# Optimization experiments

Hardware: AMD Instinct MI355X
Metric: run time of the kernel (lower is better)

## Reference

```python
import jax, jax.numpy as jnp
import numpy as np

K_DIM = 1024
HEADS = 16


def setup_inputs() -> dict:
    key = jax.random.key(0)
    ks = jax.random.split(key, 6)
    b, t, k = 2, 2048, K_DIM
    scale = 1.0 / np.sqrt(k)
    x = jax.random.normal(ks[0], (b, t, k), dtype=jnp.float32)
    # nn.Linear stores weight as [out, in]; y = x @ W.T
    Wq = jax.random.normal(ks[1], (k, k), dtype=jnp.float32) * scale
    Wk = jax.random.normal(ks[2], (k, k), dtype=jnp.float32) * scale
    Wv = jax.random.normal(ks[3], (k, k), dtype=jnp.float32) * scale
    Wo = jax.random.normal(ks[4], (k, k), dtype=jnp.float32) * scale
    bo = jax.random.normal(ks[5], (k,), dtype=jnp.float32) * scale
    return {"x": x, "Wq": Wq, "Wk": Wk, "Wv": Wv, "Wo": Wo, "bo": bo}


def reference(x, Wq, Wk, Wv, Wo, bo):
    b, t, k = x.shape
    h = HEADS
    hd = k // h
    q = (x @ Wq.T).reshape(b, t, h, hd)
    kk = (x @ Wk.T).reshape(b, t, h, hd)
    v = (x @ Wv.T).reshape(b, t, h, hd)
    # scores: [b, h, t, t]
    scores = jnp.einsum('bqhd,bkhd->bhqk', q, kk) / jnp.sqrt(jnp.float32(hd))
    w = jax.nn.softmax(scores, axis=-1)
    out = jnp.einsum('bhqk,bkhd->bqhd', w, v).reshape(b, t, k)
    return out @ Wo.T + bo
```

## Files before the change

### kernel.cpp

```cpp
#include <hip/hip_runtime.h>
#include <stdint.h>
#include <stddef.h>

#define TB 2048
#define KDIM 1024
#define NH 16
#define HD 64

typedef __attribute__((ext_vector_type(8))) __bf16 bf16x8;
typedef __attribute__((ext_vector_type(4))) float f32x4;
typedef __attribute__((ext_vector_type(16))) float f32x16;
typedef __attribute__((ext_vector_type(8))) unsigned short u16x8;
typedef __attribute__((ext_vector_type(4))) unsigned u32x4;
typedef __attribute__((ext_vector_type(2))) unsigned u32x2;

static __device__ __forceinline__ unsigned short f2bf(float f) {
  unsigned u = __builtin_bit_cast(unsigned, f);
  return (unsigned short)((u + 0x7FFFu + ((u >> 16) & 1u)) >> 16);
}

static __device__ __forceinline__ bf16x8 ld_frag(const unsigned short* p) {
  u16x8 v = *(const u16x8*)p;
  return __builtin_bit_cast(bf16x8, v);
}

static __device__ __forceinline__ void gload_lds16(const void* g, void* l) {
  auto gp = (const __attribute__((address_space(1))) unsigned int*)(uintptr_t)g;
  auto lp = (__attribute__((address_space(3))) unsigned int*)(unsigned int)(uintptr_t)l;
  __builtin_amdgcn_global_load_lds(gp, lp, 16, 0, 0);
}

static __device__ __forceinline__ float fast_exp2(float x) {
  float r;
  asm("v_exp_f32 %0, %1" : "=v"(r) : "v"(x));
  return r;
}

static __device__ __forceinline__ unsigned cvt_pk(float a, float b) {
  unsigned r;
  asm("v_cvt_pk_bf16_f32 %0, %1, %2" : "=v"(r) : "v"(a), "v"(b));
  return r;
}

static __device__ __forceinline__ u32x2 permswap(unsigned a, unsigned b) {
  return __builtin_amdgcn_permlane32_swap(a, b, false, false);
}

__global__ __launch_bounds__(256) void k_cvt_all(
    const float* __restrict__ x, const float* __restrict__ Wq,
    const float* __restrict__ Wk, const float* __restrict__ Wv,
    const float* __restrict__ Wo, unsigned short* __restrict__ xb,
    unsigned short* __restrict__ wb) {
  int bb = blockIdx.x;
  const float* src;
  unsigned short* dst;
  int i;
  if (bb < 2048) {
    src = x; dst = xb; i = bb * 256 + threadIdx.x;
  } else {
    int wsel = (bb - 2048) >> 9;
    src = (wsel == 0) ? Wq : (wsel == 1) ? Wk : (wsel == 2) ? Wv : Wo;
    dst = wb + (size_t)wsel * (KDIM * KDIM);
    i = ((bb - 2048) & 511) * 256 + threadIdx.x;
  }
  const float4* p = (const float4*)src + (size_t)i * 2;
  float4 a = p[0], b = p[1];
  u16x8 o;
  o[0] = f2bf(a.x); o[1] = f2bf(a.y); o[2] = f2bf(a.z); o[3] = f2bf(a.w);
  o[4] = f2bf(b.x); o[5] = f2bf(b.y); o[6] = f2bf(b.z); o[7] = f2bf(b.w);
  *((u16x8*)dst + i) = o;
}

template <int MODE>
static __device__ __forceinline__ void gemm_body(
    const unsigned short* __restrict__ A, const unsigned short* __restrict__ W,
    unsigned short* __restrict__ Cb, float* __restrict__ Cf,
    const float* __restrict__ bias, int by, int bx,
    unsigned short* As, unsigned short* Bs) {
  const int K = KDIM, N = KDIM;
  int tid = threadIdx.x, lane = tid & 63, wid = tid >> 6;
  int r = lane & 15, g = lane >> 4;
  int wm = wid >> 1, wn = wid & 1;

  f32x4 acc[4][4];
#pragma unroll
  for (int m = 0; m < 4; ++m)
#pragma unroll
    for (int n = 0; n < 4; ++n) acc[m][n] = (f32x4){0.f, 0.f, 0.f, 0.f};

  const unsigned short* Ag = A + (size_t)(by * 128) * K;
  const unsigned short* Wg = W + (size_t)(bx * 128) * K;

  for (int k0 = 0; k0 < K; k0 += 32) {
#pragma unroll
    for (int it = 0; it < 2; ++it) {
      int base = it * 256 + wid * 64;
      int c = base + lane;
      gload_lds16(Ag + (size_t)(c >> 2) * K + k0 + (c & 3) * 8, &As[base * 8]);
      gload_lds16(Wg + (size_t)(c >> 2) * K + k0 + (c & 3) * 8, &Bs[base * 8]);
    }
    __syncthreads();
    bf16x8 af[4], bf[4];
#pragma unroll
    for (int m = 0; m < 4; ++m) af[m] = ld_frag(&As[(wm * 64 + m * 16 + r) * 32 + g * 8]);
#pragma unroll
    for (int n = 0; n < 4; ++n) bf[n] = ld_frag(&Bs[(wn * 64 + n * 16 + r) * 32 + g * 8]);
#pragma unroll
    for (int m = 0; m < 4; ++m)
#pragma unroll
      for (int n = 0; n < 4; ++n)
        acc[m][n] = __builtin_amdgcn_mfma_f32_16x16x32_bf16(af[m], bf[n], acc[m][n], 0, 0, 0);
    __syncthreads();
  }

#pragma unroll
  for (int m = 0; m < 4; ++m)
#pragma unroll
    for (int n = 0; n < 4; ++n) {
      int col = bx * 128 + wn * 64 + n * 16 + r;
#pragma unroll
      for (int j = 0; j < 4; ++j) {
        int row = by * 128 + wm * 64 + m * 16 + g * 4 + j;
        if (MODE == 0)
          Cb[(size_t)row * N + col] = f2bf(acc[m][n][j]);
        else
          Cf[(size_t)row * N + col] = acc[m][n][j] + bias[col];
      }
    }
}

__global__ __launch_bounds__(256) void k_gemm_qkv(
    const unsigned short* __restrict__ X,
    const unsigned short* __restrict__ Wq, const unsigned short* __restrict__ Wk,
    const unsigned short* __restrict__ Wv,
    unsigned short* __restrict__ Q, unsigned short* __restrict__ Kp,
    unsigned short* __restrict__ V) {
  __shared__ __align__(16) unsigned short As[4096];
  __shared__ __align__(16) unsigned short Bs[4096];
  int idx = blockIdx.x;
  int by = idx / 24, bxx = idx % 24;
  int which = bxx >> 3, bx = bxx & 7;
  const unsigned short* W = (which == 0) ? Wq : (which == 1) ? Wk : Wv;
  unsigned short* C = (which == 0) ? Q : (which == 1) ? Kp : V;
  gemm_body<0>(X, W, C, nullptr, nullptr, by, bx, As, Bs);
}

__global__ __launch_bounds__(256) void k_gemm_out(
    const unsigned short* __restrict__ AO, const unsigned short* __restrict__ Wo,
    float* __restrict__ out, const float* __restrict__ bias) {
  __shared__ __align__(16) unsigned short As[4096];
  __shared__ __align__(16) unsigned short Bs[4096];
  int by = blockIdx.x >> 3, bx = blockIdx.x & 7;
  gemm_body<1>(AO, Wo, nullptr, out, bias, by, bx, As, Bs);
}

__global__ __launch_bounds__(256) void k_transpose_v(
    const unsigned short* __restrict__ V, unsigned short* __restrict__ Vt) {
  int tt = blockIdx.x & 31, bh = blockIdx.x >> 5;
  int b = bh >> 4, h = bh & 15;
  __shared__ __align__(16) unsigned short ls[64][72];
  int tid = threadIdx.x;
#pragma unroll
  for (int it = 0; it < 2; ++it) {
    int c = it * 256 + tid;
    int t = c >> 3, d0 = (c & 7) * 8;
    const unsigned short* src = V + ((size_t)(b * TB + tt * 64 + t)) * KDIM + h * HD + d0;
    *(u16x8*)&ls[t][d0] = *(const u16x8*)src;
  }
  __syncthreads();
#pragma unroll
  for (int it = 0; it < 2; ++it) {
    int c = it * 256 + tid;
    int d = c >> 3, t0 = (c & 7) * 8;
    u16x8 v;
#pragma unroll
    for (int j = 0; j < 8; ++j) v[j] = ls[t0 + j][d];
    unsigned short* dst = Vt + ((size_t)(bh * HD + d)) * TB + tt * 64 + t0;
    *(u16x8*)dst = v;
  }
}

__global__ __launch_bounds__(256) void k_attn(
    const unsigned short* __restrict__ Q, const unsigned short* __restrict__ Kp,
    const unsigned short* __restrict__ Vt, unsigned short* __restrict__ AO) {
  __shared__ __align__(16) unsigned short Ks[2][64 * 64];
  __shared__ __align__(16) unsigned short Vs[2][64 * 64];

  int qt = blockIdx.x & 15, bh = blockIdx.x >> 4;
  int b = bh >> 4, h = bh & 15;
  int tid = threadIdx.x, lane = tid & 63, w = tid >> 6;
  int q = lane & 31, hh = lane >> 5;
  const float LOG2E = 1.44269504f;
  const int NT = TB / 64;

  const unsigned short* Qp =
      Q + ((size_t)(b * TB + qt * 128 + w * 32 + q)) * KDIM + h * HD;
  bf16x8 qf[4];
#pragma unroll
  for (int f = 0; f < 4; ++f) qf[f] = ld_frag(&Qp[16 * f + 8 * hh]);

  f32x16 o0, o1;
#pragma unroll
  for (int i = 0; i < 16; ++i) { o0[i] = 0.f; o1[i] = 0.f; }
  float m_run = -1e30f, l_run = 0.f;

  const unsigned short* Kbase = Kp + (size_t)(b * TB) * KDIM + h * HD;
  const unsigned short* Vbase = Vt + (size_t)bh * HD * TB;

  auto stage = [&](int kt, int buf) {
#pragma unroll
    for (int it = 0; it < 2; ++it) {
      int base = it * 256 + w * 64;
      int c = base + lane;
      int rr = c >> 3;
      int blk = (c & 7) ^ (rr & 7);
      gload_lds16(Kbase + (size_t)(kt * 64 + rr) * KDIM + blk * 8, &Ks[buf][base * 8]);
      gload_lds16(Vbase + (size_t)rr * TB + kt * 64 + blk * 8, &Vs[buf][base * 8]);
    }
  };

  stage(0, 0);
  __syncthreads();
  int cur = 0;

  for (int kt = 0; kt < NT; ++kt) {
    if (kt + 1 < NT) stage(kt + 1, cur ^ 1);

    const unsigned short* Kc = &Ks[cur][0];
    f32x16 st[2];
    __builtin_amdgcn_s_setprio(1);
#pragma unroll
    for (int g = 0; g < 2; ++g) {
#pragma unroll
      for (int i = 0; i < 16; ++i) st[g][i] = 0.f;
#pragma unroll
      for (int f = 0; f < 4; ++f) {
        int row = g * 32 + q;
        int bl = (2 * f + hh) ^ (row & 7);
        bf16x8 kf = ld_frag(&Kc[row * 64 + bl * 8]);
        st[g] = __builtin_amdgcn_mfma_f32_32x32x16_bf16(kf, qf[f], st[g], 0, 0, 0);
      }
    }
    __builtin_amdgcn_s_setprio(0);

    float pm = -1e30f;
#pragma unroll
    for (int g = 0; g < 2; ++g)
#pragma unroll
      for (int i = 0; i < 16; ++i) pm = fmaxf(pm, st[g][i]);
    pm = fmaxf(pm, __shfl_xor(pm, 32));
    float spm = pm * 0.125f;
    if (!__all(spm <= m_run + 8.f)) {
      float mnew = fmaxf(m_run, spm);
      float sc = fast_exp2((m_run - mnew) * LOG2E);
      m_run = mnew;
      l_run *= sc;
#pragma unroll
      for (int p = 0; p < 16; ++p) {
        float scp = __shfl(sc, (p & 3) + 8 * (p >> 2) + 4 * hh);
        o0[p] *= scp;
        o1[p] *= scp;
      }
    }

    float c1 = 0.125f * LOG2E, c2 = m_run * LOG2E;
    float rs = 0.f;
    bf16x8 pa[4];
#pragma unroll
    for (int g = 0; g < 2; ++g) {
      float e[16];
#pragma unroll
      for (int i = 0; i < 16; ++i) {
        e[i] = fast_exp2(st[g][i] * c1 - c2);
        rs += e[i];
      }
      unsigned d[8];
#pragma unroll
      for (int i = 0; i < 8; ++i) d[i] = cvt_pk(e[2 * i], e[2 * i + 1]);
      u32x2 r1 = permswap(d[0], d[2]);
      u32x2 r2 = permswap(d[1], d[3]);
      u32x2 r3 = permswap(d[4], d[6]);
      u32x2 r4 = permswap(d[5], d[7]);
      u32x4 t0; t0[0] = r1.x; t0[1] = r2.x; t0[2] = r1.y; t0[3] = r2.y;
      u32x4 t1; t1[0] = r3.x; t1[1] = r4.x; t1[2] = r3.y; t1[3] = r4.y;
      pa[2 * g]     = __builtin_bit_cast(bf16x8, t0);
      pa[2 * g + 1] = __builtin_bit_cast(bf16x8, t1);
    }
    rs += __shfl_xor(rs, 32);
    l_run += rs;

    const unsigned short* Vc = &Vs[cur][0];
    __builtin_amdgcn_s_setprio(1);
#pragma unroll
    for (int s = 0; s < 4; ++s) {
      int bl = (2 * s + hh) ^ (q & 7);
      bf16x8 v0 = ld_frag(&Vc[q * 64 + bl * 8]);
      bf16x8 v1 = ld_frag(&Vc[(32 + q) * 64 + bl * 8]);
      o0 = __builtin_amdgcn_mfma_f32_32x32x16_bf16(pa[s], v0, o0, 0, 0, 0);
      o1 = __builtin_amdgcn_mfma_f32_32x32x16_bf16(pa[s], v1, o1, 0, 0, 0);
    }
    __builtin_amdgcn_s_setprio(0);

    __syncthreads();
    cur ^= 1;
  }

  float invl = 1.0f / l_run;
#pragma unroll
  for (int p = 0; p < 16; ++p) {
    int qr = (p & 3) + 8 * (p >> 2) + 4 * hh;
    float il = __shfl(invl, qr);
    int row = qt * 128 + w * 32 + qr;
    size_t base = ((size_t)(b * TB + row)) * KDIM + h * HD;
    AO[base + q]      = f2bf(o0[p] * il);
    AO[base + 32 + q] = f2bf(o1[p] * il);
  }
}

extern "C" void kernel_launch(void* const* d_in, const int* in_sizes, int n_in,
                              void* d_out, int out_size, void* d_ws, size_t ws_size,
                              hipStream_t stream) {
  const float* x  = (const float*)d_in[0];
  const float* Wq = (const float*)d_in[1];
  const float* Wk = (const float*)d_in[2];
  const float* Wv = (const float*)d_in[3];
  const float* Wo = (const float*)d_in[4];
  const float* bo = (const float*)d_in[5];

  char* ws = (char*)d_ws;
  const size_t MB = 1 << 20;
  unsigned short* xb  = (unsigned short*)(ws + 0 * MB);
  unsigned short* wqb = (unsigned short*)(ws + 8 * MB);
  unsigned short* wkb = (unsigned short*)(ws + 10 * MB);
  unsigned short* wvb = (unsigned short*)(ws + 12 * MB);
  unsigned short* wob = (unsigned short*)(ws + 14 * MB);
  unsigned short* Qb  = (unsigned short*)(ws + 16 * MB);
  unsigned short* Kb  = (unsigned short*)(ws + 24 * MB);
  unsigned short* Vb  = (unsigned short*)(ws + 32 * MB);
  unsigned short* Vtb = (unsigned short*)(ws + 40 * MB);
  unsigned short* AOb = (unsigned short*)(ws + 48 * MB);

  k_cvt_all<<<4096, 256, 0, stream>>>(x, Wq, Wk, Wv, Wo, xb, wqb);
  k_gemm_qkv<<<32 * 24, 256, 0, stream>>>(xb, wqb, wkb, wvb, Qb, Kb, Vb);
  k_transpose_v<<<1024, 256, 0, stream>>>(Vb, Vtb);
  k_attn<<<512, 256, 0, stream>>>(Qb, Kb, Vtb, AOb);
  k_gemm_out<<<256, 256, 0, stream>>>(AOb, wob, (float*)d_out, bo);
}
```

Before: 127.3 us.

## Split attention KV sequence across two wave groups per block and merge

```diff
diff --git a/kernel.cpp b/kernel.cpp
--- a/kernel.cpp
+++ b/kernel.cpp
@@ -180,21 +180,22 @@
   }
 }
 
-__global__ __launch_bounds__(256) void k_attn(
+__global__ __launch_bounds__(512, 4) void k_attn(
     const unsigned short* __restrict__ Q, const unsigned short* __restrict__ Kp,
     const unsigned short* __restrict__ Vt, unsigned short* __restrict__ AO) {
-  __shared__ __align__(16) unsigned short Ks[2][64 * 64];
-  __shared__ __align__(16) unsigned short Vs[2][64 * 64];
+  __shared__ __align__(16) unsigned short Ks[2][2][4096];
+  __shared__ __align__(16) unsigned short Vs[2][2][4096];
 
   int qt = blockIdx.x & 15, bh = blockIdx.x >> 4;
   int b = bh >> 4, h = bh & 15;
   int tid = threadIdx.x, lane = tid & 63, w = tid >> 6;
+  int wl = w & 3, half = w >> 2;
   int q = lane & 31, hh = lane >> 5;
   const float LOG2E = 1.44269504f;
-  const int NT = TB / 64;
+  const int HT = (TB / 64) / 2;
 
   const unsigned short* Qp =
-      Q + ((size_t)(b * TB + qt * 128 + w * 32 + q)) * KDIM + h * HD;
+      Q + ((size_t)(b * TB + qt * 128 + wl * 32 + q)) * KDIM + h * HD;
   bf16x8 qf[4];
 #pragma unroll
   for (int f = 0; f < 4; ++f) qf[f] = ld_frag(&Qp[16 * f + 8 * hh]);
@@ -210,23 +211,25 @@
   auto stage = [&](int kt, int buf) {
 #pragma unroll
     for (int it = 0; it < 2; ++it) {
-      int base = it * 256 + w * 64;
+      int base = it * 256 + wl * 64;
       int c = base + lane;
       int rr = c >> 3;
       int blk = (c & 7) ^ (rr & 7);
-      gload_lds16(Kbase + (size_t)(kt * 64 + rr) * KDIM + blk * 8, &Ks[buf][base * 8]);
-      gload_lds16(Vbase + (size_t)rr * TB + kt * 64 + blk * 8, &Vs[buf][base * 8]);
+      gload_lds16(Kbase + (size_t)(kt * 64 + rr) * KDIM + blk * 8,
+                  &Ks[half][buf][base * 8]);
+      gload_lds16(Vbase + (size_t)rr * TB + kt * 64 + blk * 8,
+                  &Vs[half][buf][base * 8]);
     }
   };
 
-  stage(0, 0);
+  stage(half * HT, 0);
   __syncthreads();
   int cur = 0;
 
-  for (int kt = 0; kt < NT; ++kt) {
-    if (kt + 1 < NT) stage(kt + 1, cur ^ 1);
-
-    const unsigned short* Kc = &Ks[cur][0];
+  for (int t = 0; t < HT; ++t) {
+    if (t + 1 < HT) stage(half * HT + t + 1, cur ^ 1);
+
+    const unsigned short* Kc = &Ks[half][cur][0];
     f32x16 st[2];
     __builtin_amdgcn_s_setprio(1);
 #pragma unroll
@@ -243,11 +246,12 @@
     }
     __builtin_amdgcn_s_setprio(0);
 
-    float pm = -1e30f;
+    float pm4[4] = {-1e30f, -1e30f, -1e30f, -1e30f};
 #pragma unroll
     for (int g = 0; g < 2; ++g)
 #pragma unroll
-      for (int i = 0; i < 16; ++i) pm = fmaxf(pm, st[g][i]);
+      for (int i = 0; i < 16; ++i) pm4[i & 3] = fmaxf(pm4[i & 3], st[g][i]);
+    float pm = fmaxf(fmaxf(pm4[0], pm4[1]), fmaxf(pm4[2], pm4[3]));
     pm = fmaxf(pm, __shfl_xor(pm, 32));
     float spm = pm * 0.125f;
     if (!__all(spm <= m_run + 8.f)) {
@@ -264,7 +268,7 @@
     }
 
     float c1 = 0.125f * LOG2E, c2 = m_run * LOG2E;
-    float rs = 0.f;
+    float rs4[4] = {0.f, 0.f, 0.f, 0.f};
     bf16x8 pa[4];
 #pragma unroll
     for (int g = 0; g < 2; ++g) {
@@ -272,7 +276,7 @@
 #pragma unroll
       for (int i = 0; i < 16; ++i) {
         e[i] = fast_exp2(st[g][i] * c1 - c2);
-        rs += e[i];
+        rs4[i & 3] += e[i];
       }
       unsigned d[8];
 #pragma unroll
@@ -286,10 +290,11 @@
       pa[2 * g]     = __builtin_bit_cast(bf16x8, t0);
       pa[2 * g + 1] = __builtin_bit_cast(bf16x8, t1);
     }
+    float rs = (rs4[0] + rs4[1]) + (rs4[2] + rs4[3]);
     rs += __shfl_xor(rs, 32);
     l_run += rs;
 
-    const unsigned short* Vc = &Vs[cur][0];
+    const unsigned short* Vc = &Vs[half][cur][0];
     __builtin_amdgcn_s_setprio(1);
 #pragma unroll
     for (int s = 0; s < 4; ++s) {
@@ -305,15 +310,39 @@
     cur ^= 1;
   }
 
-  float invl = 1.0f / l_run;
-#pragma unroll
-  for (int p = 0; p < 16; ++p) {
-    int qr = (p & 3) + 8 * (p >> 2) + 4 * hh;
-    float il = __shfl(invl, qr);
-    int row = qt * 128 + w * 32 + qr;
-    size_t base = ((size_t)(b * TB + row)) * KDIM + h * HD;
-    AO[base + q]      = f2bf(o0[p] * il);
-    AO[base + 32 + q] = f2bf(o1[p] * il);
+  float* Osw = (float*)&Vs[0][0][0];
+  float* MLb = (float*)&Ks[0][0][0];
+  if (half) {
+#pragma unroll
+    for (int p = 0; p < 16; ++p) {
+      Osw[p * 256 + wl * 64 + lane]        = o0[p];
+      Osw[(16 + p) * 256 + wl * 64 + lane] = o1[p];
+    }
+    if (!hh) {
+      MLb[wl * 32 + q]       = m_run;
+      MLb[128 + wl * 32 + q] = l_run;
+    }
+  }
+  __syncthreads();
+  if (!half) {
+    float m2 = MLb[wl * 32 + q], l2 = MLb[128 + wl * 32 + q];
+    float mm = fmaxf(m_run, m2);
+    float ea = fast_exp2((m_run - mm) * LOG2E);
+    float eb = fast_exp2((m2 - mm) * LOG2E);
+    float il = 1.f / (l_run * ea + l2 * eb);
+#pragma unroll
+    for (int p = 0; p < 16; ++p) {
+      int qr = (p & 3) + 8 * (p >> 2) + 4 * hh;
+      float a  = __shfl(ea, qr);
+      float bb = __shfl(eb, qr);
+      float ip = __shfl(il, qr);
+      float v0 = (o0[p] * a + Osw[p * 256 + wl * 64 + lane] * bb) * ip;
+      float v1 = (o1[p] * a + Osw[(16 + p) * 256 + wl * 64 + lane] * bb) * ip;
+      int row = qt * 128 + wl * 32 + qr;
+      size_t base = ((size_t)(b * TB + row)) * KDIM + h * HD;
+      AO[base + q]      = f2bf(v0);
+      AO[base + 32 + q] = f2bf(v1);
+    }
   }
 }
 
@@ -343,6 +372,6 @@
   k_cvt_all<<<4096, 256, 0, stream>>>(x, Wq, Wk, Wv, Wo, xb, wqb);
   k_gemm_qkv<<<32 * 24, 256, 0, stream>>>(xb, wqb, wkb, wvb, Qb, Kb, Vb);
   k_transpose_v<<<1024, 256, 0, stream>>>(Vb, Vtb);
-  k_attn<<<512, 256, 0, stream>>>(Qb, Kb, Vtb, AOb);
+  k_attn<<<512, 512, 0, stream>>>(Qb, Kb, Vtb, AOb);
   k_gemm_out<<<256, 256, 0, stream>>>(AOb, wob, (float*)d_out, bo);
 }
```

Measured after the change: 125.5 us. About the same (-1.5%).
